# Kernel tuning notes

Measured on AMD Instinct MI355X. Metric: run time of the kernel, lower is better.

The kernel has to match this reference:

```python
import jax, jax.numpy as jnp
import numpy as np

H = 6        # attn heads (hardcoded in DinoPool forward via view(..., 6, 64))
D = 64       # head dim
BLOCK = 512  # block-diagonal mask window (stands in for the torch BlockMask)


def setup_inputs() -> dict:
    key = jax.random.key(0)
    k1, k2, k3 = jax.random.split(key, 3)
    B, S = 4, 4096
    x = jax.random.normal(k1, (B, S, H * D), dtype=jnp.float32)
    x1 = jax.random.normal(k2, (B, S, H * D), dtype=jnp.float32)  # unused by module
    x2 = jax.random.normal(k3, (B, S, H * D), dtype=jnp.float32)  # unused by module
    # block-diagonal mask: q attends to kv within the same BLOCK-sized window
    blk = jnp.arange(S) // BLOCK
    mask = blk[:, None] == blk[None, :]  # [S, S] bool
    return {"x": x, "x1": x1, "x2": x2, "mask": mask}


def reference(x, x1, x2, mask):
    # score_mod returns score*0+1: all unmasked scores are equal, so softmax is a
    # uniform average over unmasked kv positions -> masked average pooling over V.
    B, S, _ = x.shape
    v = x.reshape(B, S, H, D).transpose(0, 2, 1, 3)          # [B, H, S, D]
    m = mask.astype(x.dtype)                                  # [S, S]
    denom = m.sum(axis=-1)                                    # [S], count of unmasked kv per q
    numer = jnp.einsum('qk,bhkd->bhqd', m, v)                 # masked sum over kv
    y = numer / denom[None, None, :, None]                    # [B, H, S, D]
    return y.transpose(0, 2, 1, 3).reshape(B, S, H * D)       # [B, S, H*D]
```

## Files before the change

### kernel.cpp

```cpp
#include <hip/hip_runtime.h>


#define BB   4
#define SS   4096
#define CC   384
#define BLK  512
#define NBLK 8
#define NT   384
#define NSUB 16
#define RWS  (BLK / NSUB)
#define CH4  (CC / 4)

__global__ __launch_bounds__(NT) void dinopool_fused(
    const float* __restrict__ x, float* __restrict__ out) {
  __shared__ float part[4][CC];
  __shared__ __align__(16) float smean[CC];

  int bid   = blockIdx.x;
  int group = bid & 31;
  int sub   = bid >> 5;
  int blk   = group & (NBLK - 1);
  int b     = group >> 3;
  int t     = threadIdx.x;
  int cq    = t % CH4;
  int g     = t / CH4;

  const float4* xv = (const float4*)(x + (size_t)(b * SS + blk * BLK) * CC);
  float a0 = 0.f, a1 = 0.f, a2 = 0.f, a3 = 0.f;
#pragma unroll 8
  for (int k = 0; k < BLK / 4; ++k) {
    float4 v = xv[(size_t)(g + 4 * k) * CH4 + cq];
    a0 += v.x; a1 += v.y; a2 += v.z; a3 += v.w;
  }
  part[g][cq * 4 + 0] = a0;
  part[g][cq * 4 + 1] = a1;
  part[g][cq * 4 + 2] = a2;
  part[g][cq * 4 + 3] = a3;
  __syncthreads();

  float s = 0.f;
#pragma unroll
  for (int gg = 0; gg < 4; ++gg) s += part[gg][t];
  smean[t] = s * (1.0f / (float)BLK);
  __syncthreads();

  const float4* sv = (const float4*)smean;
  float4* ov = (float4*)(out + (size_t)(b * SS + blk * BLK + sub * RWS) * CC);
  const int total = RWS * CH4;
  for (int i = t; i < total; i += NT) ov[i] = sv[i % CH4];
}

extern "C" void kernel_launch(void* const* d_in, const int* in_sizes, int n_in,
                              void* d_out, int out_size, void* d_ws,
                              size_t ws_size, hipStream_t stream) {
  const float* x = (const float*)d_in[0];
  float* out = (float*)d_out;
  dinopool_fused<<<BB * NBLK * NSUB, NT, 0, stream>>>(x, out);
}
```

Before: 153.0 us.

## Split pooling into column-sum and broadcast kernels to remove redundant reads

Replaces the fused kernel, in which every output sub-block re-reads the entire 512-row window, with two kernels. The first computes partial column sums over row chunks once into workspace. The second reduces those partials and broadcasts the mean to the output rows. This removes the 16x redundant reading of the input at the cost of an extra kernel launch and a small workspace round-trip.

```diff
diff --git a/kernel.cpp b/kernel.cpp
--- a/kernel.cpp
+++ b/kernel.cpp
@@ -7,28 +7,29 @@
 #define BLK  512
 #define NBLK 8
 #define NT   384
+#define RCH  8
+#define ROWS (BLK / RCH)
 #define NSUB 16
 #define RWS  (BLK / NSUB)
 #define CH4  (CC / 4)
 
-__global__ __launch_bounds__(NT) void dinopool_fused(
-    const float* __restrict__ x, float* __restrict__ out) {
+__global__ __launch_bounds__(NT) void colsum_f32(
+    const float* __restrict__ x, float* __restrict__ ws) {
   __shared__ float part[4][CC];
-  __shared__ __align__(16) float smean[CC];
 
-  int bid   = blockIdx.x;
-  int group = bid & 31;
-  int sub   = bid >> 5;
-  int blk   = group & (NBLK - 1);
-  int b     = group >> 3;
-  int t     = threadIdx.x;
-  int cq    = t % CH4;
-  int g     = t / CH4;
+  int bid = blockIdx.x;
+  int r   = bid & (RCH - 1);
+  int blk = (bid >> 3) & (NBLK - 1);
+  int b   = bid >> 6;
+  int t   = threadIdx.x;
+  int cq  = t % CH4;
+  int g   = t / CH4;
 
-  const float4* xv = (const float4*)(x + (size_t)(b * SS + blk * BLK) * CC);
+  const float4* xv =
+      (const float4*)(x + (size_t)(b * SS + blk * BLK + r * ROWS) * CC);
   float a0 = 0.f, a1 = 0.f, a2 = 0.f, a3 = 0.f;
-#pragma unroll 8
-  for (int k = 0; k < BLK / 4; ++k) {
+#pragma unroll
+  for (int k = 0; k < ROWS / 4; ++k) {
     float4 v = xv[(size_t)(g + 4 * k) * CH4 + cq];
     a0 += v.x; a1 += v.y; a2 += v.z; a3 += v.w;
   }
@@ -41,6 +42,23 @@
   float s = 0.f;
 #pragma unroll
   for (int gg = 0; gg < 4; ++gg) s += part[gg][t];
+  ws[(size_t)bid * CC + t] = s;
+}
+
+__global__ __launch_bounds__(NT) void bcast_f32(
+    const float* __restrict__ ws, float* __restrict__ out) {
+  __shared__ __align__(16) float smean[CC];
+
+  int bid = blockIdx.x;
+  int sub = bid & (NSUB - 1);
+  int blk = (bid >> 4) & (NBLK - 1);
+  int b   = bid >> 7;
+  int t   = threadIdx.x;
+
+  const float* wp = ws + (size_t)((b * NBLK + blk) * RCH) * CC + t;
+  float s = 0.0f;
+#pragma unroll
+  for (int k = 0; k < RCH; ++k) s += wp[(size_t)k * CC];
   smean[t] = s * (1.0f / (float)BLK);
   __syncthreads();
 
@@ -55,5 +73,8 @@
                               size_t ws_size, hipStream_t stream) {
   const float* x = (const float*)d_in[0];
   float* out = (float*)d_out;
-  dinopool_fused<<<BB * NBLK * NSUB, NT, 0, stream>>>(x, out);
+  float* ws = (float*)d_ws;
+
+  colsum_f32<<<BB * NBLK * RCH, NT, 0, stream>>>(x, ws);
+  bcast_f32<<<BB * NBLK * NSUB, NT, 0, stream>>>(ws, out);
 }
```

Measured after the change: 140.0 us. 8.5% less time.
